# Performance work log

Hardware: AMD Instinct MI355X
Metric: run time of the kernel (lower is better)

## Reference

```python
import jax, jax.numpy as jnp
import numpy as np

K = 3  # hardcoded kNN size in the module

def setup_inputs() -> dict:
    key = jax.random.key(0)
    ks = jax.random.split(key, 8)
    B, M, N, C, NC, OUT = 2, 4096, 8192, 512, 20, 512
    def rn(k, sh, sc=1.0):
        return jax.random.normal(k, sh, dtype=jnp.float32) * sc
    return {
        "src_points": rn(ks[0], (B, M, 3)),
        "tgt_points": rn(ks[1], (B, N, 3)),
        "src_features": rn(ks[2], (B, M, C)),
        # semantic_head: Linear(C,128) -> ReLU -> Linear(128,NC)
        "w_sem1": rn(ks[3], (C, 128), 0.04), "b_sem1": jnp.zeros((128,), jnp.float32),
        "w_sem2": rn(ks[4], (128, NC), 0.08), "b_sem2": jnp.zeros((NC,), jnp.float32),
        # upsample_net: Linear(C+NC,256) -> ReLU -> Linear(256,OUT)
        "w_up1": rn(ks[5], (C + NC, 256), 0.04), "b_up1": jnp.zeros((256,), jnp.float32),
        "w_up2": rn(ks[6], (256, OUT), 0.06), "b_up2": jnp.zeros((OUT,), jnp.float32),
    }

def reference(src_points, tgt_points, src_features,
              w_sem1, b_sem1, w_sem2, b_sem2,
              w_up1, b_up1, w_up2, b_up2):
    # semantic logits per source point: [B, M, NC]
    semantic_logits = jax.nn.relu(src_features @ w_sem1 + b_sem1) @ w_sem2 + b_sem2
    # pairwise euclidean distances tgt->src: [B, N, M]
    d2 = (jnp.sum(tgt_points * tgt_points, -1)[:, :, None]
          + jnp.sum(src_points * src_points, -1)[:, None, :]
          - 2.0 * jnp.einsum('bnd,bmd->bnm', tgt_points, src_points))
    dists = jnp.sqrt(jnp.maximum(d2, 0.0))
    # k smallest distances and their indices
    neg_vals, knn_idx = jax.lax.top_k(-dists, K)   # [B, N, K]
    knn_d = -neg_vals                               # gathered distances, [B, N, K]
    # gather neighbor features / semantics: [B, N, K, C] and [B, N, K, NC]
    knn_features = jax.vmap(lambda f, i: f[i])(src_features, knn_idx)
    knn_semantic = jax.vmap(lambda f, i: f[i])(semantic_logits, knn_idx)
    # inverse-distance softmax weights over the K neighbors
    weights = jax.nn.softmax(-knn_d, axis=-1)                       # [B, N, K]
    semantic_weights = jax.nn.softmax(knn_semantic, axis=-1).mean(axis=2)  # [B, N, NC]
    fused_features = jnp.einsum('bnkd,bnk->bnd', knn_features, weights)    # [B, N, C]
    combined = jnp.concatenate([fused_features, semantic_weights], axis=-1)
    upsampled = jax.nn.relu(combined @ w_up1 + b_up1) @ w_up2 + b_up2      # [B, N, OUT]
    return (upsampled, semantic_logits)
```

## Files before the change

kernel.cpp:

```cpp
#include <hip/hip_runtime.h>
#include <math.h>

#define BB 2
#define MM 4096
#define NN 8192
#define CC 512
#define NC 20
#define OUTD 512
#define H1 128
#define H2 256
#define CIN 532
#define KNN 3
#define SPLIT 32
#define CHUNK (MM / SPLIT)
#define CLEN (CHUNK / 4)

#define RR 32
#define HS 264
#define KT2 8
#define KT1 17

#define RO 16
#define FS 520
#define HS2 136
#define TS 512
#define SKT1 16
#define SKT2 4

#define NPREP 544
#define NKNNB (BB * NN / 512 * SPLIT)
#define NSEMB (BB * MM / RO)

typedef __attribute__((ext_vector_type(8))) short s8;
typedef __attribute__((ext_vector_type(4))) float f4;

__device__ inline unsigned short f2bf(float x) {
    unsigned u = __float_as_uint(x);
    unsigned r = (u + 0x7FFFu + ((u >> 16) & 1u)) >> 16;
    return (unsigned short)r;
}
__device__ inline float bf2fs(short u) {
    return __uint_as_float(((unsigned)(unsigned short)u) << 16);
}

__global__ __launch_bounds__(256) void prep_kernel(
    const float* __restrict__ srcp,
    const float* __restrict__ wu1, const float* __restrict__ wu2,
    const float* __restrict__ ws1, const float* __restrict__ ws2,
    float4* __restrict__ sp4,
    unsigned short* __restrict__ w1p, unsigned short* __restrict__ w2p,
    unsigned short* __restrict__ ws1p, unsigned short* __restrict__ ws2p)
{
    int i = blockIdx.x * 256 + threadIdx.x;
    if (i < BB * MM) {
        float x = srcp[(size_t)i * 3 + 0];
        float y = srcp[(size_t)i * 3 + 1];
        float z = srcp[(size_t)i * 3 + 2];
        sp4[i] = make_float4(x, y, z, x * x + y * y + z * z);
    }
    if (i < KT1 * H2 * 32) {
        int kk = i & 31, n = (i >> 5) & 255, kb = i >> 13;
        int k = kb * 32 + kk;
        w1p[i] = f2bf((k < CIN) ? wu1[(size_t)k * H2 + n] : 0.0f);
    }
    if (i < KT2 * OUTD * 32) {
        int kk = i & 31, n = (i >> 5) & 511, kb = i >> 14;
        int k = kb * 32 + kk;
        w2p[i] = f2bf(wu2[(size_t)k * OUTD + n]);
    }
    if (i < SKT1 * H1 * 32) {
        int kk = i & 31, n = (i >> 5) & 127, kb = i >> 12;
        int k = kb * 32 + kk;
        ws1p[i] = f2bf(ws1[(size_t)k * H1 + n]);
    }
    if (i < SKT2 * 32 * 32) {
        int kk = i & 31, n = (i >> 5) & 31, kb = i >> 10;
        int k = kb * 32 + kk;
        ws2p[i] = f2bf((n < NC) ? ws2[(size_t)k * NC + n] : 0.0f);
    }
}

__global__ __launch_bounds__(512) void fused_kernel(
    const float4* __restrict__ sp4, const float* __restrict__ tgtp,
    float* __restrict__ pd2, unsigned short* __restrict__ pidx,
    const float* __restrict__ feat,
    const unsigned short* __restrict__ ws1p, const unsigned short* __restrict__ ws2p,
    const unsigned short* __restrict__ w1p,
    const float* __restrict__ b1s, const float* __restrict__ b2s,
    float* __restrict__ logits_out, unsigned short* __restrict__ T)
{
    __shared__ __align__(16) char smem[24128];
    const int tid = threadIdx.x;
    const int bx = blockIdx.x;

    if (bx >= NSEMB) {
        const int idx = bx - NSEMB;
        const int g = idx & 31;
        const int chunk = idx >> 5;
        const int t = g * 512 + tid;
        const int bu = g >> 4;
        const int mbase = chunk * CHUNK;
        const float4* sp = sp4 + (size_t)bu * MM + mbase;

        const float tx = tgtp[(size_t)t * 3 + 0];
        const float ty = tgtp[(size_t)t * 3 + 1];
        const float tz = tgtp[(size_t)t * 3 + 2];
        const float m2x = -2.0f * tx, m2y = -2.0f * ty, m2z = -2.0f * tz;

        float b0[4], b1[4], b2[4];
        int i0[4], i1[4], i2[4];
#pragma unroll
        for (int k = 0; k < 4; ++k) {
            b0[k] = b1[k] = b2[k] = 1e30f;
            i0[k] = i1[k] = i2[k] = 0;
        }

#pragma unroll 4
        for (int m = 0; m < CLEN; ++m) {
#pragma unroll
            for (int k = 0; k < 4; ++k) {
                float4 p = sp[k * CLEN + m];
                float d = fmaf(m2x, p.x, fmaf(m2y, p.y, fmaf(m2z, p.z, p.w)));
                int mi = mbase + k * CLEN + m;
                bool l2 = d < b2[k], l1 = d < b1[k], l0 = d < b0[k];
                i2[k] = l1 ? i1[k] : (l2 ? mi : i2[k]);
                i1[k] = l0 ? i0[k] : (l1 ? mi : i1[k]);
                i0[k] = l0 ? mi : i0[k];
                b2[k] = __builtin_amdgcn_fmed3f(d, b1[k], b2[k]);
                b1[k] = __builtin_amdgcn_fmed3f(d, b0[k], b1[k]);
                b0[k] = fminf(d, b0[k]);
            }
        }
#pragma unroll
        for (int k = 1; k < 4; ++k) {
#pragma unroll
            for (int j = 0; j < 3; ++j) {
                float d = (j == 0) ? b0[k] : (j == 1) ? b1[k] : b2[k];
                int   i = (j == 0) ? i0[k] : (j == 1) ? i1[k] : i2[k];
                bool e2 = d < b2[0], e1 = d < b1[0], e0 = d < b0[0];
                i2[0] = e1 ? i1[0] : (e2 ? i : i2[0]);
                i1[0] = e0 ? i0[0] : (e1 ? i : i1[0]);
                i0[0] = e0 ? i : i0[0];
                b2[0] = __builtin_amdgcn_fmed3f(d, b1[0], b2[0]);
                b1[0] = __builtin_amdgcn_fmed3f(d, b0[0], b1[0]);
                b0[0] = fminf(d, b0[0]);
            }
        }
        size_t o = ((size_t)t * SPLIT + chunk) * KNN;
        pd2[o + 0] = b0[0]; pd2[o + 1] = b1[0]; pd2[o + 2] = b2[0];
        pidx[o + 0] = (unsigned short)i0[0];
        pidx[o + 1] = (unsigned short)i1[0];
        pidx[o + 2] = (unsigned short)i2[0];
        return;
    }

    unsigned short* sfeat = (unsigned short*)smem;
    unsigned short* Tst   = (unsigned short*)smem;
    unsigned short* shid  = (unsigned short*)(smem + 16640);
    float*          slg   = (float*)(smem + 20992);
    unsigned short* pP    = (unsigned short*)(smem + 23104);
    const int row0 = bx * RO;
    const int lane = tid & 63;
    const int wv = tid >> 6;
    const int l15 = lane & 15;
    const int quad = lane >> 4;

    {
        const int r = tid >> 5, p = tid & 31;
        const float4* fr = (const float4*)(feat + (size_t)(row0 + r) * CC);
#pragma unroll
        for (int j = 0; j < 4; ++j) {
            int c4 = j * 32 + p;
            float4 a = fr[c4];
            ushort4 s;
            s.x = f2bf(a.x); s.y = f2bf(a.y); s.z = f2bf(a.z); s.w = f2bf(a.w);
            *(ushort4*)&sfeat[r * FS + c4 * 4] = s;
        }
    }
    __syncthreads();

    f4 asem, ah[2];
    {
        asem = (f4){0.f, 0.f, 0.f, 0.f};
#pragma unroll
        for (int c = 0; c < 2; ++c) ah[c] = (f4){0.f, 0.f, 0.f, 0.f};
        for (int kb = 0; kb < SKT1; ++kb) {
            s8 a = *(const s8*)&sfeat[l15 * FS + kb * 32 + quad * 8];
            {
                s8 b = *(const s8*)&ws1p[((size_t)(kb * H1 + wv * 16 + l15)) * 32 + quad * 8];
                asem = __builtin_amdgcn_mfma_f32_16x16x32_bf16(a, b, asem, 0, 0, 0);
            }
#pragma unroll
            for (int c = 0; c < 2; ++c) {
                s8 b = *(const s8*)&w1p[((size_t)(kb * H2 + wv * 32 + c * 16 + l15)) * 32 + quad * 8];
                ah[c] = __builtin_amdgcn_mfma_f32_16x16x32_bf16(a, b, ah[c], 0, 0, 0);
            }
        }
    }
    __syncthreads();
    {
        {
            int col = wv * 16 + l15;
            float bias = b1s[col];
#pragma unroll
            for (int i = 0; i < 4; ++i) {
                int rr = quad * 4 + i;
                shid[rr * HS2 + col] = f2bf(fmaxf(asem[i] + bias, 0.0f));
            }
        }
#pragma unroll
        for (int c = 0; c < 2; ++c) {
            int col = wv * 32 + c * 16 + l15;
#pragma unroll
            for (int i = 0; i < 4; ++i) {
                int rr = quad * 4 + i;
                Tst[rr * TS + col] = f2bf(ah[c][i]);
            }
        }
    }
    __syncthreads();

    if (wv < 2) {
        f4 acc = (f4){0.f, 0.f, 0.f, 0.f};
        for (int kb = 0; kb < SKT2; ++kb) {
            s8 a = *(const s8*)&shid[l15 * HS2 + kb * 32 + quad * 8];
            s8 b = *(const s8*)&ws2p[((size_t)(kb * 32 + wv * 16 + l15)) * 32 + quad * 8];
            acc = __builtin_amdgcn_mfma_f32_16x16x32_bf16(a, b, acc, 0, 0, 0);
        }
        int col = wv * 16 + l15;
        float bias = (col < NC) ? b2s[col] : 0.0f;
#pragma unroll
        for (int i = 0; i < 4; ++i) {
            int rr = quad * 4 + i;
            float v = acc[i] + bias;
            slg[rr * 33 + col] = v;
            if (col < NC)
                logits_out[(size_t)(row0 + rr) * NC + col] = v;
        }
    }
    __syncthreads();

    if (tid < RO) {
        int r = tid;
        float mx = -1e30f;
        for (int nc = 0; nc < NC; ++nc) mx = fmaxf(mx, slg[r * 33 + nc]);
        float s = 0.0f;
        float e[NC];
#pragma unroll
        for (int nc = 0; nc < NC; ++nc) { e[nc] = __expf(slg[r * 33 + nc] - mx); s += e[nc]; }
        float inv = 1.0f / s;
#pragma unroll
        for (int nc = 0; nc < 32; ++nc)
            pP[r * 32 + nc] = (nc < NC) ? f2bf(e[nc] * inv) : 0;
    }
    __syncthreads();

    {
        s8 a = *(const s8*)&pP[l15 * 32 + quad * 8];
#pragma unroll
        for (int c = 0; c < 2; ++c) {
            s8 b = *(const s8*)&w1p[((size_t)(16 * H2 + wv * 32 + c * 16 + l15)) * 32 + quad * 8];
            f4 acc = (f4){0.f, 0.f, 0.f, 0.f};
            acc = __builtin_amdgcn_mfma_f32_16x16x32_bf16(a, b, acc, 0, 0, 0);
            int col = wv * 32 + c * 16 + l15;
#pragma unroll
            for (int i = 0; i < 4; ++i) {
                int rr = quad * 4 + i;
                Tst[rr * TS + 256 + col] = f2bf(acc[i]);
            }
        }
    }
    __syncthreads();

    {
#pragma unroll
        for (int v = 0; v < 2; ++v) {
            int e = (tid + v * 512) * 8;
            int r = e >> 9, c = e & (TS - 1);
            s8 d = *(const s8*)&Tst[e];
            *(s8*)&T[((size_t)(row0 + r)) * TS + c] = d;
        }
    }
}

__global__ __launch_bounds__(256) void up_kernel(
    const unsigned short* __restrict__ T,
    const float* __restrict__ pd2, const unsigned short* __restrict__ pidx,
    const float* __restrict__ tgtp,
    const unsigned short* __restrict__ w2p,
    const float* __restrict__ b1g, const float* __restrict__ b2g,
    float* __restrict__ out)
{
    __shared__ unsigned short hid[RR * HS];
    __shared__ float sg[RR][3];
    __shared__ int   sj[RR][3];
    __shared__ float pb[RR][4][3];
    __shared__ int   pi[RR][4][3];
    const int tid = threadIdx.x;
    const int row0 = blockIdx.x * RR;
    const int lane = tid & 63;
    const int wv = tid >> 6;
    const int l15 = lane & 15;
    const int quad = lane >> 4;

    if (tid < RR * 4) {
        const int r = tid >> 2, p = tid & 3;
        int row = row0 + r;
        float b0 = 1e30f, b1 = 1e30f, b2 = 1e30f;
        int i0 = 0, i1 = 0, i2 = 0;
        size_t base = (size_t)row * SPLIT * KNN + (size_t)p * 8 * KNN;
#pragma unroll
        for (int j = 0; j < 8 * KNN; ++j) {
            float d = pd2[base + j];
            int m = pidx[base + j];
            bool l2 = d < b2, l1 = d < b1, l0 = d < b0;
            i2 = l1 ? i1 : (l2 ? m : i2);
            i1 = l0 ? i0 : (l1 ? m : i1);
            i0 = l0 ? m : i0;
            b2 = __builtin_amdgcn_fmed3f(d, b1, b2);
            b1 = __builtin_amdgcn_fmed3f(d, b0, b1);
            b0 = fminf(d, b0);
        }
        pb[r][p][0] = b0; pb[r][p][1] = b1; pb[r][p][2] = b2;
        pi[r][p][0] = i0; pi[r][p][1] = i1; pi[r][p][2] = i2;
    }
    __syncthreads();

    if (tid < RR) {
        int row = row0 + tid;
        float b0 = 1e30f, b1 = 1e30f, b2 = 1e30f;
        int i0 = 0, i1 = 0, i2 = 0;
#pragma unroll
        for (int p = 0; p < 4; ++p)
#pragma unroll
            for (int j = 0; j < 3; ++j) {
                float d = pb[tid][p][j];
                int m = pi[tid][p][j];
                bool l2 = d < b2, l1 = d < b1, l0 = d < b0;
                i2 = l1 ? i1 : (l2 ? m : i2);
                i1 = l0 ? i0 : (l1 ? m : i1);
                i0 = l0 ? m : i0;
                b2 = __builtin_amdgcn_fmed3f(d, b1, b2);
                b1 = __builtin_amdgcn_fmed3f(d, b0, b1);
                b0 = fminf(d, b0);
            }
        float tx = tgtp[(size_t)row * 3 + 0];
        float ty = tgtp[(size_t)row * 3 + 1];
        float tz = tgtp[(size_t)row * 3 + 2];
        float t2 = tx * tx + ty * ty + tz * tz;
        float d0 = sqrtf(fmaxf(b0 + t2, 0.0f));
        float d1 = sqrtf(fmaxf(b1 + t2, 0.0f));
        float d2v = sqrtf(fmaxf(b2 + t2, 0.0f));
        float e1 = __expf(d0 - d1);
        float e2 = __expf(d0 - d2v);
        float inv = 1.0f / (1.0f + e1 + e2);
        sg[tid][0] = inv; sg[tid][1] = e1 * inv; sg[tid][2] = e2 * inv;
        sj[tid][0] = i0; sj[tid][1] = i1; sj[tid][2] = i2;
    }
    __syncthreads();

    {
        const int r = tid >> 3, p = tid & 7, c0 = p * 32;
        int row = row0 + r;
        size_t bofs = (size_t)(row >> 13) * MM;
        float pre[32];
#pragma unroll
        for (int cc = 0; cc < 32; ++cc) pre[cc] = 0.0f;
#pragma unroll
        for (int k = 0; k < 3; ++k) {
            const unsigned short* Tr = T + (bofs + (size_t)sj[r][k]) * TS;
            float gk = sg[r][k];
#pragma unroll
            for (int v = 0; v < 4; ++v) {
                s8 h = *(const s8*)&Tr[c0 + v * 8];
                s8 g = *(const s8*)&Tr[256 + c0 + v * 8];
#pragma unroll
                for (int e = 0; e < 8; ++e) {
                    pre[v * 8 + e] = fmaf(gk, bf2fs(h[e]), pre[v * 8 + e]);
                    pre[v * 8 + e] = fmaf(1.0f / 3.0f, bf2fs(g[e]), pre[v * 8 + e]);
                }
            }
        }
#pragma unroll
        for (int cc = 0; cc < 32; ++cc) {
            int c = c0 + cc;
            hid[r * HS + c] = f2bf(fmaxf(pre[cc] + b1g[c], 0.0f));
        }
    }
    __syncthreads();

    {
        const int m0 = wv * 128;
        f4 acc2[2][8];
#pragma unroll
        for (int rt = 0; rt < 2; ++rt)
#pragma unroll
            for (int c = 0; c < 8; ++c) acc2[rt][c] = (f4){0.f, 0.f, 0.f, 0.f};
        for (int kb = 0; kb < KT2; ++kb) {
            s8 a0 = *(const s8*)&hid[l15 * HS + kb * 32 + quad * 8];
            s8 a1 = *(const s8*)&hid[(l15 + 16) * HS + kb * 32 + quad * 8];
            s8 bfr[8];
#pragma unroll
            for (int c = 0; c < 8; ++c)
                bfr[c] = *(const s8*)&w2p[((size_t)(kb * OUTD + m0 + c * 16 + l15)) * 32 + quad * 8];
#pragma unroll
            for (int c = 0; c < 8; ++c) {
                acc2[0][c] = __builtin_amdgcn_mfma_f32_16x16x32_bf16(a0, bfr[c], acc2[0][c], 0, 0, 0);
                acc2[1][c] = __builtin_amdgcn_mfma_f32_16x16x32_bf16(a1, bfr[c], acc2[1][c], 0, 0, 0);
            }
        }
#pragma unroll
        for (int c = 0; c < 8; ++c) {
            int ccol = m0 + c * 16 + l15;
            float bias = b2g[ccol];
#pragma unroll
            for (int rt = 0; rt < 2; ++rt)
#pragma unroll
                for (int i = 0; i < 4; ++i) {
                    int rr = rt * 16 + quad * 4 + i;
                    out[(size_t)(row0 + rr) * OUTD + ccol] = acc2[rt][c][i] + bias;
                }
        }
    }
}

extern "C" void kernel_launch(void* const* d_in, const int* in_sizes, int n_in,
                              void* d_out, int out_size, void* d_ws, size_t ws_size,
                              hipStream_t stream) {
    (void)in_sizes; (void)n_in; (void)out_size; (void)ws_size;
    const float* src_points   = (const float*)d_in[0];
    const float* tgt_points   = (const float*)d_in[1];
    const float* src_features = (const float*)d_in[2];
    const float* w_sem1 = (const float*)d_in[3];
    const float* b_sem1 = (const float*)d_in[4];
    const float* w_sem2 = (const float*)d_in[5];
    const float* b_sem2 = (const float*)d_in[6];
    const float* w_up1  = (const float*)d_in[7];
    const float* b_up1  = (const float*)d_in[8];
    const float* w_up2  = (const float*)d_in[9];
    const float* b_up2  = (const float*)d_in[10];

    float* out    = (float*)d_out;
    float* ups    = out;
    float* logits = out + (size_t)BB * NN * OUTD;

    char* w = (char*)d_ws;
    unsigned short* T = (unsigned short*)w;    w += (size_t)BB * MM * TS * 2;
    float* pd2  = (float*)w;                   w += (size_t)BB * NN * SPLIT * KNN * 4;
    unsigned short* pidx = (unsigned short*)w; w += (size_t)BB * NN * SPLIT * KNN * 2;
    float4* sp4 = (float4*)w;                  w += (size_t)BB * MM * 16;
    unsigned short* w1p  = (unsigned short*)w; w += (size_t)KT1 * H2 * 32 * 2;
    unsigned short* w2p  = (unsigned short*)w; w += (size_t)KT2 * OUTD * 32 * 2;
    unsigned short* ws1p = (unsigned short*)w; w += (size_t)SKT1 * H1 * 32 * 2;
    unsigned short* ws2p = (unsigned short*)w; w += (size_t)SKT2 * 32 * 32 * 2;

    prep_kernel<<<dim3(NPREP), dim3(256), 0, stream>>>(
        src_points, w_up1, w_up2, w_sem1, w_sem2, sp4, w1p, w2p, ws1p, ws2p);
    fused_kernel<<<dim3(NSEMB + NKNNB), dim3(512), 0, stream>>>(
        sp4, tgt_points, pd2, pidx,
        src_features, ws1p, ws2p, w1p, b_sem1, b_sem2, logits, T);
    up_kernel<<<dim3(BB * NN / RR), dim3(256), 0, stream>>>(
        T, pd2, pidx, tgt_points, w2p, b_up1, b_up2, ups);
}
```

Before: 157.3 us.

## Stage kNN source chunk in LDS and process two targets per thread

The kNN branch now loads each block's chunk of source points into shared memory once and reads from LDS with a one-step software prefetch, instead of each thread streaming them from global memory. Each thread now handles two target points against two interleaved sub-streams, which halves the number of kNN blocks and reuses every loaded point twice. This reduces global and cache traffic and increases instruction-level parallelism, at the cost of more registers, a block-wide barrier, and half as many blocks to spread across CUs.

```diff
diff --git a/kernel.cpp b/kernel.cpp
--- a/kernel.cpp
+++ b/kernel.cpp
@@ -13,7 +13,7 @@
 #define KNN 3
 #define SPLIT 32
 #define CHUNK (MM / SPLIT)
-#define CLEN (CHUNK / 4)
+#define HLEN (CHUNK / 2)
 
 #define RR 32
 #define HS 264
@@ -28,7 +28,7 @@
 #define SKT2 4
 
 #define NPREP 544
-#define NKNNB (BB * NN / 512 * SPLIT)
+#define NKNNB (BB * NN / 1024 * SPLIT)
 #define NSEMB (BB * MM / RO)
 
 typedef __attribute__((ext_vector_type(8))) short s8;
@@ -94,63 +94,108 @@
     const int bx = blockIdx.x;
 
     if (bx >= NSEMB) {
+        float4* pts = (float4*)smem;
         const int idx = bx - NSEMB;
-        const int g = idx & 31;
-        const int chunk = idx >> 5;
-        const int t = g * 512 + tid;
-        const int bu = g >> 4;
+        const int g = idx & 15;
+        const int chunk = idx >> 4;
+        const int ta = g * 1024 + tid;
+        const int tb = ta + 512;
+        const int bu = g >> 3;
         const int mbase = chunk * CHUNK;
-        const float4* sp = sp4 + (size_t)bu * MM + mbase;
-
-        const float tx = tgtp[(size_t)t * 3 + 0];
-        const float ty = tgtp[(size_t)t * 3 + 1];
-        const float tz = tgtp[(size_t)t * 3 + 2];
-        const float m2x = -2.0f * tx, m2y = -2.0f * ty, m2z = -2.0f * tz;
-
-        float b0[4], b1[4], b2[4];
-        int i0[4], i1[4], i2[4];
-#pragma unroll
-        for (int k = 0; k < 4; ++k) {
-            b0[k] = b1[k] = b2[k] = 1e30f;
-            i0[k] = i1[k] = i2[k] = 0;
-        }
-
-#pragma unroll 4
-        for (int m = 0; m < CLEN; ++m) {
-#pragma unroll
-            for (int k = 0; k < 4; ++k) {
-                float4 p = sp[k * CLEN + m];
-                float d = fmaf(m2x, p.x, fmaf(m2y, p.y, fmaf(m2z, p.z, p.w)));
-                int mi = mbase + k * CLEN + m;
-                bool l2 = d < b2[k], l1 = d < b1[k], l0 = d < b0[k];
-                i2[k] = l1 ? i1[k] : (l2 ? mi : i2[k]);
-                i1[k] = l0 ? i0[k] : (l1 ? mi : i1[k]);
-                i0[k] = l0 ? mi : i0[k];
-                b2[k] = __builtin_amdgcn_fmed3f(d, b1[k], b2[k]);
-                b1[k] = __builtin_amdgcn_fmed3f(d, b0[k], b1[k]);
-                b0[k] = fminf(d, b0[k]);
-            }
-        }
-#pragma unroll
-        for (int k = 1; k < 4; ++k) {
-#pragma unroll
-            for (int j = 0; j < 3; ++j) {
-                float d = (j == 0) ? b0[k] : (j == 1) ? b1[k] : b2[k];
-                int   i = (j == 0) ? i0[k] : (j == 1) ? i1[k] : i2[k];
-                bool e2 = d < b2[0], e1 = d < b1[0], e0 = d < b0[0];
-                i2[0] = e1 ? i1[0] : (e2 ? i : i2[0]);
-                i1[0] = e0 ? i0[0] : (e1 ? i : i1[0]);
-                i0[0] = e0 ? i : i0[0];
-                b2[0] = __builtin_amdgcn_fmed3f(d, b1[0], b2[0]);
-                b1[0] = __builtin_amdgcn_fmed3f(d, b0[0], b1[0]);
-                b0[0] = fminf(d, b0[0]);
-            }
-        }
-        size_t o = ((size_t)t * SPLIT + chunk) * KNN;
-        pd2[o + 0] = b0[0]; pd2[o + 1] = b1[0]; pd2[o + 2] = b2[0];
-        pidx[o + 0] = (unsigned short)i0[0];
-        pidx[o + 1] = (unsigned short)i1[0];
-        pidx[o + 2] = (unsigned short)i2[0];
+
+        if (tid < CHUNK)
+            pts[tid] = sp4[(size_t)bu * MM + mbase + tid];
+        __syncthreads();
+
+        const float ax = tgtp[(size_t)ta * 3 + 0];
+        const float ay = tgtp[(size_t)ta * 3 + 1];
+        const float az = tgtp[(size_t)ta * 3 + 2];
+        const float bxc = tgtp[(size_t)tb * 3 + 0];
+        const float byc = tgtp[(size_t)tb * 3 + 1];
+        const float bzc = tgtp[(size_t)tb * 3 + 2];
+        const float a2x = -2.0f * ax, a2y = -2.0f * ay, a2z = -2.0f * az;
+        const float b2x = -2.0f * bxc, b2y = -2.0f * byc, b2z = -2.0f * bzc;
+
+        float A0[2], A1[2], A2[2], B0[2], B1[2], B2[2];
+        int Ai0[2], Ai1[2], Ai2[2], Bi0[2], Bi1[2], Bi2[2];
+#pragma unroll
+        for (int k = 0; k < 2; ++k) {
+            A0[k] = A1[k] = A2[k] = 1e30f; B0[k] = B1[k] = B2[k] = 1e30f;
+            Ai0[k] = Ai1[k] = Ai2[k] = 0;  Bi0[k] = Bi1[k] = Bi2[k] = 0;
+        }
+
+        float4 pf0 = pts[0];
+        float4 pf1 = pts[HLEN];
+#pragma unroll 2
+        for (int m = 0; m < HLEN; ++m) {
+            float4 p0 = pf0, p1 = pf1;
+            if (m + 1 < HLEN) {
+                pf0 = pts[m + 1];
+                pf1 = pts[HLEN + m + 1];
+            }
+#pragma unroll
+            for (int k = 0; k < 2; ++k) {
+                float4 p = (k == 0) ? p0 : p1;
+                int mi = mbase + k * HLEN + m;
+                {
+                    float d = fmaf(a2x, p.x, fmaf(a2y, p.y, fmaf(a2z, p.z, p.w)));
+                    bool l2 = d < A2[k], l1 = d < A1[k], l0 = d < A0[k];
+                    Ai2[k] = l1 ? Ai1[k] : (l2 ? mi : Ai2[k]);
+                    Ai1[k] = l0 ? Ai0[k] : (l1 ? mi : Ai1[k]);
+                    Ai0[k] = l0 ? mi : Ai0[k];
+                    A2[k] = __builtin_amdgcn_fmed3f(d, A1[k], A2[k]);
+                    A1[k] = __builtin_amdgcn_fmed3f(d, A0[k], A1[k]);
+                    A0[k] = fminf(d, A0[k]);
+                }
+                {
+                    float d = fmaf(b2x, p.x, fmaf(b2y, p.y, fmaf(b2z, p.z, p.w)));
+                    bool l2 = d < B2[k], l1 = d < B1[k], l0 = d < B0[k];
+                    Bi2[k] = l1 ? Bi1[k] : (l2 ? mi : Bi2[k]);
+                    Bi1[k] = l0 ? Bi0[k] : (l1 ? mi : Bi1[k]);
+                    Bi0[k] = l0 ? mi : Bi0[k];
+                    B2[k] = __builtin_amdgcn_fmed3f(d, B1[k], B2[k]);
+                    B1[k] = __builtin_amdgcn_fmed3f(d, B0[k], B1[k]);
+                    B0[k] = fminf(d, B0[k]);
+                }
+            }
+        }
+#pragma unroll
+        for (int j = 0; j < 3; ++j) {
+            {
+                float d = (j == 0) ? A0[1] : (j == 1) ? A1[1] : A2[1];
+                int   i = (j == 0) ? Ai0[1] : (j == 1) ? Ai1[1] : Ai2[1];
+                bool e1 = d < A1[0], e0 = d < A0[0];
+                bool e2 = d < A2[0];
+                Ai2[0] = e1 ? Ai1[0] : (e2 ? i : Ai2[0]);
+                Ai1[0] = e0 ? Ai0[0] : (e1 ? i : Ai1[0]);
+                Ai0[0] = e0 ? i : Ai0[0];
+                A2[0] = __builtin_amdgcn_fmed3f(d, A1[0], A2[0]);
+                A1[0] = __builtin_amdgcn_fmed3f(d, A0[0], A1[0]);
+                A0[0] = fminf(d, A0[0]);
+            }
+            {
+                float d = (j == 0) ? B0[1] : (j == 1) ? B1[1] : B2[1];
+                int   i = (j == 0) ? Bi0[1] : (j == 1) ? Bi1[1] : Bi2[1];
+                bool e1 = d < B1[0], e0 = d < B0[0];
+                bool e2 = d < B2[0];
+                Bi2[0] = e1 ? Bi1[0] : (e2 ? i : Bi2[0]);
+                Bi1[0] = e0 ? Bi0[0] : (e1 ? i : Bi1[0]);
+                Bi0[0] = e0 ? i : Bi0[0];
+                B2[0] = __builtin_amdgcn_fmed3f(d, B1[0], B2[0]);
+                B1[0] = __builtin_amdgcn_fmed3f(d, B0[0], B1[0]);
+                B0[0] = fminf(d, B0[0]);
+            }
+        }
+        size_t oa = ((size_t)ta * SPLIT + chunk) * KNN;
+        pd2[oa + 0] = A0[0]; pd2[oa + 1] = A1[0]; pd2[oa + 2] = A2[0];
+        pidx[oa + 0] = (unsigned short)Ai0[0];
+        pidx[oa + 1] = (unsigned short)Ai1[0];
+        pidx[oa + 2] = (unsigned short)Ai2[0];
+        size_t ob = ((size_t)tb * SPLIT + chunk) * KNN;
+        pd2[ob + 0] = B0[0]; pd2[ob + 1] = B1[0]; pd2[ob + 2] = B2[0];
+        pidx[ob + 0] = (unsigned short)Bi0[0];
+        pidx[ob + 1] = (unsigned short)Bi1[0];
+        pidx[ob + 2] = (unsigned short)Bi2[0];
         return;
     }
 
```

New measurement: 161.1 us. 1.02x slower.
